# Kernel optimization log

Hardware: AMD Instinct MI355X
Metric: run time of the kernel (lower is better)

Reference implementation:

```python
import jax, jax.numpy as jnp
import numpy as np

BS = 2
EMBED = 256
NH = 8
NL = 4
NP = 4
HD = EMBED // NH
SHAPES = [(128, 128), (64, 64), (32, 32), (16, 16)]
NQ = sum(h * w for h, w in SHAPES)  # 21760


def setup_inputs() -> dict:
    key = jax.random.key(0)
    ks = jax.random.split(key, 12)
    s = 1.0 / np.sqrt(EMBED)
    return {
        "query": jax.random.normal(ks[0], (BS, NQ, EMBED), jnp.float32),
        "reference_points": jax.random.uniform(ks[1], (BS, NQ, NL, 2), jnp.float32),
        "value": jax.random.normal(ks[2], (BS, NQ, EMBED), jnp.float32),
        "W_off": jax.random.normal(ks[3], (EMBED, NH * NL * NP * 2), jnp.float32) * 0.01,
        "b_off": jax.random.normal(ks[4], (NH * NL * NP * 2,), jnp.float32) * 0.5,
        "W_attn": jax.random.normal(ks[5], (EMBED, NH * NL * NP), jnp.float32) * 0.02,
        "b_attn": jnp.zeros((NH * NL * NP,), jnp.float32),
        "W_v": jax.random.normal(ks[6], (EMBED, EMBED), jnp.float32) * s,
        "b_v": jnp.zeros((EMBED,), jnp.float32),
        "W_out": jax.random.normal(ks[7], (EMBED, EMBED), jnp.float32) * s,
        "b_out": jnp.zeros((EMBED,), jnp.float32),
        "value_spatial_shapes": np.asarray(SHAPES, dtype=np.int64),
    }


def _ms_deform_attn(value, shapes, loc, aw):
    # value: [bs,V,nh,d]; loc: [bs,nq,nh,L,P,2] in [0,1]; aw: [bs,nq,nh,L,P]
    bs, V, nh, d = value.shape
    nq = loc.shape[1]
    out = jnp.zeros((bs, nq, nh, d), value.dtype)
    start = 0
    b_idx = jnp.arange(bs)[:, None, None, None]
    h_idx = jnp.arange(nh)[None, None, :, None]
    for l, (H, W) in enumerate(shapes):
        H, W = int(H), int(W)
        v = value[:, start:start + H * W].reshape(bs, H, W, nh, d)
        start += H * W
        g = 2.0 * loc[:, :, :, l] - 1.0  # [bs,nq,nh,P,2], grid_sample convention
        # align_corners=False pixel coordinates
        x = ((g[..., 0] + 1.0) * W - 1.0) * 0.5
        y = ((g[..., 1] + 1.0) * H - 1.0) * 0.5
        x0 = jnp.floor(x); y0 = jnp.floor(y)
        wx1 = x - x0; wx0 = 1.0 - wx1
        wy1 = y - y0; wy0 = 1.0 - wy1

        def gather(yi, xi):
            inb = (yi >= 0) & (yi < H) & (xi >= 0) & (xi < W)
            yc = jnp.clip(yi, 0, H - 1).astype(jnp.int32)
            xc = jnp.clip(xi, 0, W - 1).astype(jnp.int32)
            vals = v[b_idx, yc, xc, h_idx]  # [bs,nq,nh,P,d]
            return vals * inb[..., None].astype(v.dtype)

        samp = (gather(y0, x0) * (wy0 * wx0)[..., None]
                + gather(y0, x0 + 1) * (wy0 * wx1)[..., None]
                + gather(y0 + 1, x0) * (wy1 * wx0)[..., None]
                + gather(y0 + 1, x0 + 1) * (wy1 * wx1)[..., None])
        out = out + jnp.einsum('bqhpd,bqhp->bqhd', samp, aw[:, :, :, l])
    return out.reshape(bs, nq, nh * d)


def reference(query, reference_points, value, W_off, b_off, W_attn, b_attn,
              W_v, b_v, W_out, b_out, value_spatial_shapes):
    shapes = np.asarray(value_spatial_shapes)  # static [L,2]
    bs, nq, _ = query.shape
    v = (value @ W_v + b_v).reshape(bs, -1, NH, HD)
    off = (query @ W_off + b_off).reshape(bs, nq, NH, NL, NP, 2)
    aw = (query @ W_attn + b_attn).reshape(bs, nq, NH, NL * NP)
    aw = jax.nn.softmax(aw, axis=-1).reshape(bs, nq, NH, NL, NP)
    # offset normalizer: (W,H) per level
    norm = jnp.asarray(shapes[:, ::-1].astype(np.float32))  # [L,2]
    loc = reference_points[:, :, None, :, None, :] + off / norm[None, None, None, :, None, :]
    out = _ms_deform_attn(v, shapes, loc, aw)
    return out @ W_out + b_out
```

## Files before the change

### kernel.cpp

```cpp
#include <hip/hip_runtime.h>
#include <math.h>

#define BS 2
#define NQ 21760
#define V_LEN 21760
#define EMBED 256
#define NH 8
#define NL 4
#define NP 4
#define HD 32

typedef __bf16 bf16;
typedef __bf16 bf16x8 __attribute__((ext_vector_type(8)));
typedef __bf16 bf16x4 __attribute__((ext_vector_type(4)));
typedef float f32x4 __attribute__((ext_vector_type(4)));

__global__ __launch_bounds__(256) void cast_wt(const float* __restrict__ W,
                                               bf16* __restrict__ WT, int N)
{
    int id = blockIdx.x * 256 + threadIdx.x;
    int n = id >> 8, k = id & 255;
    WT[id] = (bf16)W[k * N + n];
}

__global__ __launch_bounds__(384) void concat_bias(const float* __restrict__ b_off,
                                                   const float* __restrict__ b_attn,
                                                   float* __restrict__ bc)
{
    int id = threadIdx.x;
    bc[id] = (id < 256) ? b_off[id] : b_attn[id - 256];
}

template<bool A_BF16, bool OUT_BF16>
__global__ __launch_bounds__(256) void gemm_mfma(
    const void* __restrict__ Av, const bf16* __restrict__ WT,
    const float* __restrict__ bias, void* __restrict__ Cv,
    int N, int K, int ntn)
{
    const int bnt = blockIdx.x % ntn;
    const int bmt = blockIdx.x / ntn;
    const int bm = bmt * 128, bn = bnt * 128;

    __shared__ __align__(16) bf16 As[128][40];
    __shared__ __align__(16) bf16 Bs[128][40];

    const int tid = threadIdx.x;
    const int lane = tid & 63, wv = tid >> 6;
    const int wr = wv >> 1, wc = wv & 1;
    const int quad = lane >> 4, l16 = lane & 15;

    f32x4 acc[4][4];
    #pragma unroll
    for (int i = 0; i < 4; i++)
        #pragma unroll
        for (int j = 0; j < 4; j++)
            acc[i][j] = (f32x4){0.f, 0.f, 0.f, 0.f};

    for (int k0 = 0; k0 < K; k0 += 32) {
        if constexpr (A_BF16) {
            const bf16* A = (const bf16*)Av;
            #pragma unroll
            for (int i = 0; i < 2; i++) {
                int row = (tid >> 2) + i * 64, seg = tid & 3;
                bf16x8 v = *(const bf16x8*)&A[(size_t)(bm + row) * K + k0 + seg * 8];
                *(bf16x8*)&As[row][seg * 8] = v;
            }
        } else {
            const float* A = (const float*)Av;
            #pragma unroll
            for (int i = 0; i < 4; i++) {
                int row = (tid >> 3) + i * 32, f4 = tid & 7;
                float4 f = *(const float4*)&A[(size_t)(bm + row) * K + k0 + f4 * 4];
                bf16x4 h;
                h[0] = (bf16)f.x; h[1] = (bf16)f.y; h[2] = (bf16)f.z; h[3] = (bf16)f.w;
                *(bf16x4*)&As[row][f4 * 4] = h;
            }
        }
        #pragma unroll
        for (int i = 0; i < 2; i++) {
            int row = (tid >> 2) + i * 64, seg = tid & 3;
            bf16x8 v = *(const bf16x8*)&WT[(size_t)(bn + row) * K + k0 + seg * 8];
            *(bf16x8*)&Bs[row][seg * 8] = v;
        }
        __syncthreads();

        bf16x8 af[4], bfr[4];
        #pragma unroll
        for (int mi = 0; mi < 4; mi++)
            af[mi] = *(const bf16x8*)&As[wr * 64 + mi * 16 + l16][quad * 8];
        #pragma unroll
        for (int ni = 0; ni < 4; ni++)
            bfr[ni] = *(const bf16x8*)&Bs[wc * 64 + ni * 16 + l16][quad * 8];
        #pragma unroll
        for (int mi = 0; mi < 4; mi++)
            #pragma unroll
            for (int ni = 0; ni < 4; ni++)
                acc[mi][ni] = __builtin_amdgcn_mfma_f32_16x16x32_bf16(
                    af[mi], bfr[ni], acc[mi][ni], 0, 0, 0);
        __syncthreads();
    }

    #pragma unroll
    for (int mi = 0; mi < 4; mi++) {
        #pragma unroll
        for (int ni = 0; ni < 4; ni++) {
            const int col = bn + wc * 64 + ni * 16 + l16;
            const int row0 = bm + wr * 64 + mi * 16 + quad * 4;
            const float bc = bias[col];
            #pragma unroll
            for (int r = 0; r < 4; r++) {
                float v = acc[mi][ni][r] + bc;
                if constexpr (OUT_BF16)
                    ((bf16*)Cv)[(size_t)(row0 + r) * N + col] = (bf16)v;
                else
                    ((float*)Cv)[(size_t)(row0 + r) * N + col] = v;
            }
        }
    }
}

__global__ __launch_bounds__(64) void deform_sample(
    const bf16* __restrict__ vproj, const float* __restrict__ offaw,
    const float* __restrict__ refp, bf16* __restrict__ sampled)
{
    const int q = blockIdx.x;
    const int b = blockIdx.y;
    const int bq = b * NQ + q;
    const int t = threadIdx.x;

    __shared__ float s_off[256];
    __shared__ float s_aw[128];
    __shared__ __align__(16) float s_w[128][4];
    __shared__ __align__(16) int   s_idx[128][4];

    const float* row = offaw + (size_t)bq * 384;
    #pragma unroll
    for (int i = 0; i < 4; i++) s_off[t + i * 64] = row[t + i * 64];
    #pragma unroll
    for (int i = 0; i < 2; i++) s_aw[t + i * 64] = row[256 + t + i * 64];
    __syncthreads();

    if (t < 8) {
        float m = -1e30f;
        #pragma unroll
        for (int i = 0; i < 16; i++) m = fmaxf(m, s_aw[t * 16 + i]);
        float ssum = 0.f;
        #pragma unroll
        for (int i = 0; i < 16; i++) {
            float e = __expf(s_aw[t * 16 + i] - m);
            s_aw[t * 16 + i] = e;
            ssum += e;
        }
        float r = 1.0f / ssum;
        #pragma unroll
        for (int i = 0; i < 16; i++) s_aw[t * 16 + i] *= r;
    }
    __syncthreads();

    #pragma unroll
    for (int sI = 0; sI < 2; sI++) {
        int s = t + sI * 64;
        int h = s >> 4, lp = s & 15, l = lp >> 2, p = lp & 3;
        int Wl = 128 >> l, Hl = 128 >> l;
        int st = (l == 0) ? 0 : (l == 1) ? 16384 : (l == 2) ? 20480 : 21504;
        float rx = refp[((size_t)bq * 4 + l) * 2 + 0];
        float ry = refp[((size_t)bq * 4 + l) * 2 + 1];
        float ox = s_off[((h * NL + l) * NP + p) * 2 + 0];
        float oy = s_off[((h * NL + l) * NP + p) * 2 + 1];
        float fW = (float)Wl, fH = (float)Hl;
        float x = (rx + ox / fW) * fW - 0.5f;
        float y = (ry + oy / fH) * fH - 0.5f;
        float xf = floorf(x), yf = floorf(y);
        int x0 = (int)xf, y0 = (int)yf;
        float wx1 = x - xf, wx0 = 1.f - wx1;
        float wy1 = y - yf, wy0 = 1.f - wy1;
        float aw = s_aw[h * 16 + lp];
        bool vx0 = (x0 >= 0) && (x0 < Wl);
        bool vx1 = (x0 + 1 >= 0) && (x0 + 1 < Wl);
        bool vy0 = (y0 >= 0) && (y0 < Hl);
        bool vy1 = (y0 + 1 >= 0) && (y0 + 1 < Hl);
        int cx0 = min(max(x0, 0), Wl - 1), cx1 = min(max(x0 + 1, 0), Wl - 1);
        int cy0 = min(max(y0, 0), Hl - 1), cy1 = min(max(y0 + 1, 0), Hl - 1);
        int d = lp * 8 + h;
        s_idx[d][0] = st + cy0 * Wl + cx0;  s_w[d][0] = (vy0 && vx0) ? wy0 * wx0 * aw : 0.f;
        s_idx[d][1] = st + cy0 * Wl + cx1;  s_w[d][1] = (vy0 && vx1) ? wy0 * wx1 * aw : 0.f;
        s_idx[d][2] = st + cy1 * Wl + cx0;  s_w[d][2] = (vy1 && vx0) ? wy1 * wx0 * aw : 0.f;
        s_idx[d][3] = st + cy1 * Wl + cx1;  s_w[d][3] = (vy1 && vx1) ? wy1 * wx1 * aw : 0.f;
    }
    __syncthreads();

    const int h = t >> 3;
    const int choff = t * 4;
    const bf16* vbc = vproj + (size_t)b * V_LEN * EMBED + choff;
    float a0 = 0.f, a1 = 0.f, a2 = 0.f, a3 = 0.f;
    #pragma unroll 4
    for (int lp = 0; lp < 16; lp++) {
        const int d = lp * 8 + h;
        const float4 w4 = *(const float4*)&s_w[d][0];
        const int4  i4 = *(const int4*)&s_idx[d][0];
        bf16x4 v0 = *(const bf16x4*)(vbc + (i4.x << 8));
        bf16x4 v1 = *(const bf16x4*)(vbc + (i4.y << 8));
        bf16x4 v2 = *(const bf16x4*)(vbc + (i4.z << 8));
        bf16x4 v3 = *(const bf16x4*)(vbc + (i4.w << 8));
        a0 += w4.x * (float)v0[0] + w4.y * (float)v1[0] + w4.z * (float)v2[0] + w4.w * (float)v3[0];
        a1 += w4.x * (float)v0[1] + w4.y * (float)v1[1] + w4.z * (float)v2[1] + w4.w * (float)v3[1];
        a2 += w4.x * (float)v0[2] + w4.y * (float)v1[2] + w4.z * (float)v2[2] + w4.w * (float)v3[2];
        a3 += w4.x * (float)v0[3] + w4.y * (float)v1[3] + w4.z * (float)v2[3] + w4.w * (float)v3[3];
    }

    bf16x4 o;
    o[0] = (bf16)a0; o[1] = (bf16)a1; o[2] = (bf16)a2; o[3] = (bf16)a3;
    *(bf16x4*)&sampled[(size_t)bq * 256 + choff] = o;
}

extern "C" void kernel_launch(void* const* d_in, const int* in_sizes, int n_in,
                              void* d_out, int out_size, void* d_ws, size_t ws_size,
                              hipStream_t stream)
{
    const float* query  = (const float*)d_in[0];
    const float* refp   = (const float*)d_in[1];
    const float* value  = (const float*)d_in[2];
    const float* W_off  = (const float*)d_in[3];
    const float* b_off  = (const float*)d_in[4];
    const float* W_attn = (const float*)d_in[5];
    const float* b_attn = (const float*)d_in[6];
    const float* W_v    = (const float*)d_in[7];
    const float* b_v    = (const float*)d_in[8];
    const float* W_out  = (const float*)d_in[9];
    const float* b_out  = (const float*)d_in[10];
    float* out = (float*)d_out;

    const int M = BS * NQ;

    char* ws = (char*)d_ws;
    bf16*  WTv   = (bf16*)ws;                      ws += 256 * 256 * 2;
    bf16*  WToa  = (bf16*)ws;                      ws += 384 * 256 * 2;
    bf16*  WTu   = (bf16*)ws;                      ws += 256 * 256 * 2;
    float* bcat  = (float*)ws;                     ws += 384 * 4;
    bf16*  vproj = (bf16*)ws;                      ws += (size_t)M * 256 * 2;
    float* offaw = (float*)ws;                     ws += (size_t)M * 384 * 4;
    bf16*  samp  = (bf16*)ws;                      ws += (size_t)M * 256 * 2;

    cast_wt<<<256, 256, 0, stream>>>(W_v,   WTv, 256);
    cast_wt<<<256, 256, 0, stream>>>(W_off, WToa, 256);
    cast_wt<<<128, 256, 0, stream>>>(W_attn, WToa + 256 * 256, 128);
    cast_wt<<<256, 256, 0, stream>>>(W_out, WTu, 256);
    concat_bias<<<1, 384, 0, stream>>>(b_off, b_attn, bcat);

    gemm_mfma<false, true><<<(M / 128) * 2, 256, 0, stream>>>(value, WTv, b_v, vproj, 256, 256, 2);
    gemm_mfma<false, false><<<(M / 128) * 3, 256, 0, stream>>>(query, WToa, bcat, offaw, 384, 256, 3);
    deform_sample<<<dim3(NQ, BS), dim3(64), 0, stream>>>(vproj, offaw, refp, samp);
    gemm_mfma<true, false><<<(M / 128) * 2, 256, 0, stream>>>(samp, WTu, b_out, out, 256, 256, 2);
}
```

Measured before the change: 299.9 us.

## Use direct global-to-LDS loads in GEMM and pack four queries per sampling block

The GEMM kernel now fills shared memory with global_load_lds 16-byte transfers instead of register round-trips. For fp32 inputs it stores the raw floats with an XOR swizzle and converts them to bf16 when reading fragments, and the LDS row padding is removed. The deformable sampling kernel now processes four queries per 256-thread block, computes the softmax with wave shuffles instead of 8 serial threads, and swizzles the offset buffer to cut bank conflicts. Risks are extra LDS traffic for the fp32 A tiles, bank conflicts on the unpadded bf16 tiles, and higher LDS use per sampling block, which may reduce occupancy.

```diff
diff --git a/kernel.cpp b/kernel.cpp
--- a/kernel.cpp
+++ b/kernel.cpp
@@ -15,6 +15,11 @@
 typedef __bf16 bf16x4 __attribute__((ext_vector_type(4)));
 typedef float f32x4 __attribute__((ext_vector_type(4)));
 
+#define GLOAD_LDS16(gp, lp_) \
+    __builtin_amdgcn_global_load_lds( \
+        (const __attribute__((address_space(1))) unsigned int*)(gp), \
+        (__attribute__((address_space(3))) unsigned int*)(lp_), 16, 0, 0)
+
 __global__ __launch_bounds__(256) void cast_wt(const float* __restrict__ W,
                                                bf16* __restrict__ WT, int N)
 {
@@ -31,7 +36,7 @@
     bc[id] = (id < 256) ? b_off[id] : b_attn[id - 256];
 }
 
-template<bool A_BF16, bool OUT_BF16>
+template<bool A_F32, bool OUT_BF16>
 __global__ __launch_bounds__(256) void gemm_mfma(
     const void* __restrict__ Av, const bf16* __restrict__ WT,
     const float* __restrict__ bias, void* __restrict__ Cv,
@@ -41,8 +46,9 @@
     const int bmt = blockIdx.x / ntn;
     const int bm = bmt * 128, bn = bnt * 128;
 
-    __shared__ __align__(16) bf16 As[128][40];
-    __shared__ __align__(16) bf16 Bs[128][40];
+    __shared__ __align__(16) bf16 Bs[128 * 32];
+    __shared__ __align__(16) unsigned char AsRaw[A_F32 ? 128 * 32 * 4
+                                                       : 128 * 32 * 2];
 
     const int tid = threadIdx.x;
     const int lane = tid & 63, wv = tid >> 6;
@@ -56,41 +62,63 @@
         for (int j = 0; j < 4; j++)
             acc[i][j] = (f32x4){0.f, 0.f, 0.f, 0.f};
 
+    const int b_row = tid >> 2, b_chunk = tid & 3;
+    const int a_row8 = tid >> 3, a_phys = tid & 7;
+
     for (int k0 = 0; k0 < K; k0 += 32) {
-        if constexpr (A_BF16) {
+        if constexpr (A_F32) {
+            const float* A = (const float*)Av;
+            #pragma unroll
+            for (int p = 0; p < 4; p++) {
+                int row = a_row8 + p * 32;
+                int csrc = a_phys ^ (row & 7);
+                GLOAD_LDS16(&A[(size_t)(bm + row) * K + k0 + csrc * 4],
+                            AsRaw + p * 4096 + tid * 16);
+            }
+        } else {
             const bf16* A = (const bf16*)Av;
             #pragma unroll
-            for (int i = 0; i < 2; i++) {
-                int row = (tid >> 2) + i * 64, seg = tid & 3;
-                bf16x8 v = *(const bf16x8*)&A[(size_t)(bm + row) * K + k0 + seg * 8];
-                *(bf16x8*)&As[row][seg * 8] = v;
+            for (int p = 0; p < 2; p++) {
+                int row = b_row + p * 64;
+                GLOAD_LDS16(&A[(size_t)(bm + row) * K + k0 + b_chunk * 8],
+                            AsRaw + p * 4096 + tid * 16);
+            }
+        }
+        #pragma unroll
+        for (int p = 0; p < 2; p++) {
+            int row = b_row + p * 64;
+            GLOAD_LDS16(&WT[(size_t)(bn + row) * K + k0 + b_chunk * 8],
+                        (unsigned char*)Bs + p * 4096 + tid * 16);
+        }
+        __syncthreads();
+
+        bf16x8 af[4], bfr[4];
+        if constexpr (A_F32) {
+            const float* Asf = (const float*)AsRaw;
+            #pragma unroll
+            for (int mi = 0; mi < 4; mi++) {
+                int r = wr * 64 + mi * 16 + l16;
+                int g = r & 7;
+                f32x4 u0 = *(const f32x4*)&Asf[r * 32 + ((2 * quad) ^ g) * 4];
+                f32x4 u1 = *(const f32x4*)&Asf[r * 32 + ((2 * quad + 1) ^ g) * 4];
+                bf16x8 h;
+                h[0] = (bf16)u0[0]; h[1] = (bf16)u0[1]; h[2] = (bf16)u0[2]; h[3] = (bf16)u0[3];
+                h[4] = (bf16)u1[0]; h[5] = (bf16)u1[1]; h[6] = (bf16)u1[2]; h[7] = (bf16)u1[3];
+                af[mi] = h;
             }
         } else {
-            const float* A = (const float*)Av;
-            #pragma unroll
-            for (int i = 0; i < 4; i++) {
-                int row = (tid >> 3) + i * 32, f4 = tid & 7;
-                float4 f = *(const float4*)&A[(size_t)(bm + row) * K + k0 + f4 * 4];
-                bf16x4 h;
-                h[0] = (bf16)f.x; h[1] = (bf16)f.y; h[2] = (bf16)f.z; h[3] = (bf16)f.w;
-                *(bf16x4*)&As[row][f4 * 4] = h;
-            }
-        }
-        #pragma unroll
-        for (int i = 0; i < 2; i++) {
-            int row = (tid >> 2) + i * 64, seg = tid & 3;
-            bf16x8 v = *(const bf16x8*)&WT[(size_t)(bn + row) * K + k0 + seg * 8];
-            *(bf16x8*)&Bs[row][seg * 8] = v;
-        }
-        __syncthreads();
-
-        bf16x8 af[4], bfr[4];
-        #pragma unroll
-        for (int mi = 0; mi < 4; mi++)
-            af[mi] = *(const bf16x8*)&As[wr * 64 + mi * 16 + l16][quad * 8];
-        #pragma unroll
-        for (int ni = 0; ni < 4; ni++)
-            bfr[ni] = *(const bf16x8*)&Bs[wc * 64 + ni * 16 + l16][quad * 8];
+            const bf16* Asb = (const bf16*)AsRaw;
+            #pragma unroll
+            for (int mi = 0; mi < 4; mi++) {
+                int r = wr * 64 + mi * 16 + l16;
+                af[mi] = *(const bf16x8*)&Asb[r * 32 + quad * 8];
+            }
+        }
+        #pragma unroll
+        for (int ni = 0; ni < 4; ni++) {
+            int r = wc * 64 + ni * 16 + l16;
+            bfr[ni] = *(const bf16x8*)&Bs[r * 32 + quad * 8];
+        }
         #pragma unroll
         for (int mi = 0; mi < 4; mi++)
             #pragma unroll
@@ -119,54 +147,62 @@
     }
 }
 
-__global__ __launch_bounds__(64) void deform_sample(
+__global__ __launch_bounds__(256) void deform_sample(
     const bf16* __restrict__ vproj, const float* __restrict__ offaw,
     const float* __restrict__ refp, bf16* __restrict__ sampled)
 {
-    const int q = blockIdx.x;
+    const int wv = threadIdx.x >> 6;
+    const int t = threadIdx.x & 63;
+    const int q = blockIdx.x * 4 + wv;
     const int b = blockIdx.y;
     const int bq = b * NQ + q;
-    const int t = threadIdx.x;
-
-    __shared__ float s_off[256];
-    __shared__ float s_aw[128];
-    __shared__ __align__(16) float s_w[128][4];
-    __shared__ __align__(16) int   s_idx[128][4];
+
+    __shared__ __align__(16) float s_off[4][256];
+    __shared__ __align__(16) float s_aw[4][128];
+    __shared__ __align__(16) float s_w[4][128][4];
+    __shared__ __align__(16) int   s_idx[4][128][4];
 
     const float* row = offaw + (size_t)bq * 384;
     #pragma unroll
-    for (int i = 0; i < 4; i++) s_off[t + i * 64] = row[t + i * 64];
-    #pragma unroll
-    for (int i = 0; i < 2; i++) s_aw[t + i * 64] = row[256 + t + i * 64];
+    for (int i = 0; i < 4; i++) {
+        int j = t + i * 64;
+        s_off[wv][j ^ (((j >> 5) & 7) << 2)] = row[j];
+    }
+    #pragma unroll
+    for (int i = 0; i < 2; i++) s_aw[wv][t + i * 64] = row[256 + t + i * 64];
     __syncthreads();
 
-    if (t < 8) {
-        float m = -1e30f;
-        #pragma unroll
-        for (int i = 0; i < 16; i++) m = fmaxf(m, s_aw[t * 16 + i]);
-        float ssum = 0.f;
-        #pragma unroll
-        for (int i = 0; i < 16; i++) {
-            float e = __expf(s_aw[t * 16 + i] - m);
-            s_aw[t * 16 + i] = e;
-            ssum += e;
-        }
-        float r = 1.0f / ssum;
-        #pragma unroll
-        for (int i = 0; i < 16; i++) s_aw[t * 16 + i] *= r;
+    {
+        const int h = t >> 3, e = t & 7;
+        float v0 = s_aw[wv][h * 16 + e];
+        float v1 = s_aw[wv][h * 16 + 8 + e];
+        float m = fmaxf(v0, v1);
+        m = fmaxf(m, __shfl_xor(m, 1));
+        m = fmaxf(m, __shfl_xor(m, 2));
+        m = fmaxf(m, __shfl_xor(m, 4));
+        float e0 = __expf(v0 - m), e1 = __expf(v1 - m);
+        float ssum = e0 + e1;
+        ssum += __shfl_xor(ssum, 1);
+        ssum += __shfl_xor(ssum, 2);
+        ssum += __shfl_xor(ssum, 4);
+        float rs = 1.0f / ssum;
+        s_aw[wv][h * 16 + e] = e0 * rs;
+        s_aw[wv][h * 16 + 8 + e] = e1 * rs;
     }
     __syncthreads();
 
     #pragma unroll
     for (int sI = 0; sI < 2; sI++) {
-        int s = t + sI * 64;
-        int h = s >> 4, lp = s & 15, l = lp >> 2, p = lp & 3;
+        int h = t & 7;
+        int lp = (t >> 3) + sI * 8;
+        int l = lp >> 2, p = lp & 3;
         int Wl = 128 >> l, Hl = 128 >> l;
         int st = (l == 0) ? 0 : (l == 1) ? 16384 : (l == 2) ? 20480 : 21504;
         float rx = refp[((size_t)bq * 4 + l) * 2 + 0];
         float ry = refp[((size_t)bq * 4 + l) * 2 + 1];
-        float ox = s_off[((h * NL + l) * NP + p) * 2 + 0];
-        float oy = s_off[((h * NL + l) * NP + p) * 2 + 1];
+        int j = h * 32 + lp * 2;
+        float2 oxy = *(const float2*)&s_off[wv][j ^ (h << 2)];
+        float ox = oxy.x, oy = oxy.y;
         float fW = (float)Wl, fH = (float)Hl;
         float x = (rx + ox / fW) * fW - 0.5f;
         float y = (ry + oy / fH) * fH - 0.5f;
@@ -174,7 +210,7 @@
         int x0 = (int)xf, y0 = (int)yf;
         float wx1 = x - xf, wx0 = 1.f - wx1;
         float wy1 = y - yf, wy0 = 1.f - wy1;
-        float aw = s_aw[h * 16 + lp];
+        float aw = s_aw[wv][h * 16 + lp];
         bool vx0 = (x0 >= 0) && (x0 < Wl);
         bool vx1 = (x0 + 1 >= 0) && (x0 + 1 < Wl);
         bool vy0 = (y0 >= 0) && (y0 < Hl);
@@ -182,10 +218,10 @@
         int cx0 = min(max(x0, 0), Wl - 1), cx1 = min(max(x0 + 1, 0), Wl - 1);
         int cy0 = min(max(y0, 0), Hl - 1), cy1 = min(max(y0 + 1, 0), Hl - 1);
         int d = lp * 8 + h;
-        s_idx[d][0] = st + cy0 * Wl + cx0;  s_w[d][0] = (vy0 && vx0) ? wy0 * wx0 * aw : 0.f;
-        s_idx[d][1] = st + cy0 * Wl + cx1;  s_w[d][1] = (vy0 && vx1) ? wy0 * wx1 * aw : 0.f;
-        s_idx[d][2] = st + cy1 * Wl + cx0;  s_w[d][2] = (vy1 && vx0) ? wy1 * wx0 * aw : 0.f;
-        s_idx[d][3] = st + cy1 * Wl + cx1;  s_w[d][3] = (vy1 && vx1) ? wy1 * wx1 * aw : 0.f;
+        s_idx[wv][d][0] = st + cy0 * Wl + cx0;  s_w[wv][d][0] = (vy0 && vx0) ? wy0 * wx0 * aw : 0.f;
+        s_idx[wv][d][1] = st + cy0 * Wl + cx1;  s_w[wv][d][1] = (vy0 && vx1) ? wy0 * wx1 * aw : 0.f;
+        s_idx[wv][d][2] = st + cy1 * Wl + cx0;  s_w[wv][d][2] = (vy1 && vx0) ? wy1 * wx0 * aw : 0.f;
+        s_idx[wv][d][3] = st + cy1 * Wl + cx1;  s_w[wv][d][3] = (vy1 && vx1) ? wy1 * wx1 * aw : 0.f;
     }
     __syncthreads();
 
@@ -196,8 +232,8 @@
     #pragma unroll 4
     for (int lp = 0; lp < 16; lp++) {
         const int d = lp * 8 + h;
-        const float4 w4 = *(const float4*)&s_w[d][0];
-        const int4  i4 = *(const int4*)&s_idx[d][0];
+        const float4 w4 = *(const float4*)&s_w[wv][d][0];
+        const int4  i4 = *(const int4*)&s_idx[wv][d][0];
         bf16x4 v0 = *(const bf16x4*)(vbc + (i4.x << 8));
         bf16x4 v1 = *(const bf16x4*)(vbc + (i4.y << 8));
         bf16x4 v2 = *(const bf16x4*)(vbc + (i4.z << 8));
@@ -247,8 +283,8 @@
     cast_wt<<<256, 256, 0, stream>>>(W_out, WTu, 256);
     concat_bias<<<1, 384, 0, stream>>>(b_off, b_attn, bcat);
 
-    gemm_mfma<false, true><<<(M / 128) * 2, 256, 0, stream>>>(value, WTv, b_v, vproj, 256, 256, 2);
-    gemm_mfma<false, false><<<(M / 128) * 3, 256, 0, stream>>>(query, WToa, bcat, offaw, 384, 256, 3);
-    deform_sample<<<dim3(NQ, BS), dim3(64), 0, stream>>>(vproj, offaw, refp, samp);
-    gemm_mfma<true, false><<<(M / 128) * 2, 256, 0, stream>>>(samp, WTu, b_out, out, 256, 256, 2);
-}
+    gemm_mfma<true, true><<<(M / 128) * 2, 256, 0, stream>>>(value, WTv, b_v, vproj, 256, 256, 2);
+    gemm_mfma<true, false><<<(M / 128) * 3, 256, 0, stream>>>(query, WToa, bcat, offaw, 384, 256, 3);
+    deform_sample<<<dim3(NQ / 4, BS), dim3(256), 0, stream>>>(vproj, offaw, refp, samp);
+    gemm_mfma<false, false><<<(M / 128) * 2, 256, 0, stream>>>(samp, WTu, b_out, out, 256, 256, 2);
+}
```

Measured after the change: 304.7 us. Within noise of the previous version (+1.6%).
